# Performance work log

Measured on AMD Instinct MI355X. Metric: run time of the kernel, lower is better.

The kernel has to match this reference:

```python
import jax, jax.numpy as jnp
import numpy as np

B, N, K, CLS = 256, 15, 520, 800  # batch, points per streamline, k+k_global, classes
EPS = 1e-5


def _bn(x, g, b, m, v, axis=1):
    # eval-mode BatchNorm with running stats
    shape = [1] * x.ndim
    shape[axis] = -1
    rs = lambda a: a.reshape(shape)
    return rs(g) * (x - rs(m)) * jax.lax.rsqrt(rs(v) + EPS) + rs(b)


def setup_inputs():
    key = jax.random.key(0)
    kit = iter(jax.random.split(key, 24))
    nk = lambda: next(kit)
    p = {}
    p["pts"] = jax.random.normal(nk(), (B, N, 3), jnp.float32)
    p["label"] = jax.random.randint(nk(), (B,), 0, CLS)
    p["info_point_set"] = jax.random.normal(nk(), (B, K, N, 3), jnp.float32)

    def lin(cout, cin):
        w = jax.random.normal(nk(), (cout, cin), jnp.float32) * (1.0 / np.sqrt(cin))
        return w, jnp.zeros((cout,), jnp.float32)

    def bn(c):
        return (jnp.ones((c,), jnp.float32), jnp.zeros((c,), jnp.float32),
                jax.random.normal(nk(), (c,), jnp.float32) * 0.05,
                jnp.ones((c,), jnp.float32))

    p["w_info"], p["b_info"] = lin(64, 6)
    p["g_info"], p["be_info"], p["m_info"], p["v_info"] = bn(64)
    p["w2"], p["b2"] = lin(128, 64)
    p["g2"], p["be2"], p["m2"], p["v2"] = bn(128)
    p["w3"], p["b3"] = lin(1024, 128)
    p["g3"], p["be3"], p["m3"], p["v3"] = bn(1024)
    p["wf1"], p["bf1"] = lin(512, 1024)
    p["gf1"], p["bef1"], p["mf1"], p["vf1"] = bn(512)
    p["wf2"], p["bf2"] = lin(256, 512)
    p["gf2"], p["bef2"], p["mf2"], p["vf2"] = bn(256)
    p["wf3"], p["bf3"] = lin(CLS, 256)
    return p


def reference(pts, label, info_point_set,
              w_info, b_info, g_info, be_info, m_info, v_info,
              w2, b2, g2, be2, m2, v2,
              w3, b3, g3, be3, m3, v3,
              wf1, bf1, gf1, bef1, mf1, vf1,
              wf2, bf2, gf2, bef2, mf2, vf2,
              wf3, bf3):
    x = jnp.transpose(pts, (0, 2, 1))                      # [B,3,N]
    ips = jnp.transpose(info_point_set, (0, 3, 2, 1))      # [B,3,N,K]
    xr = jnp.broadcast_to(x[..., None], ips.shape)         # [B,3,N,K]
    h = jnp.concatenate([ips - xr, xr], axis=1)            # [B,6,N,K]
    h = jnp.einsum('oc,bcnk->bonk', w_info, h) + b_info[None, :, None, None]
    h = jax.nn.relu(_bn(h, g_info, be_info, m_info, v_info))
    h = jnp.max(h, axis=-1)                                # [B,64,N]  (max over neighbors)
    h2 = jax.nn.relu(_bn(jnp.einsum('oc,bcn->bon', w2, h) + b2[None, :, None],
                         g2, be2, m2, v2))                 # [B,128,N]
    h3 = _bn(jnp.einsum('oc,bcn->bon', w3, h2) + b3[None, :, None],
             g3, be3, m3, v3)                              # [B,1024,N]
    g = jnp.max(h3, axis=2)                                # [B,1024] global max-pool
    f1 = jax.nn.relu(_bn(g @ wf1.T + bf1, gf1, bef1, mf1, vf1, axis=1))
    f2 = jax.nn.relu(_bn(f1 @ wf2.T + bf2, gf2, bef2, mf2, vf2, axis=1))  # dropout identity (eval)
    ret = f2 @ wf3.T + bf3                                 # [B,CLS]
    return (ret, f2)
```

## Files before the change

kernel.cpp:

```cpp
#include <hip/hip_runtime.h>
#include <math.h>

#define EPS 1e-5f

typedef __attribute__((ext_vector_type(8))) short short8v;
typedef __attribute__((ext_vector_type(4))) float f32x4;
typedef __attribute__((ext_vector_type(16))) float f32x16;

__device__ __forceinline__ unsigned short bf16r(float x) {
    unsigned u = __float_as_uint(x);
    return (unsigned short)((u + 0x7FFFu + ((u >> 16) & 1u)) >> 16);
}
__device__ __forceinline__ float bf2f(unsigned short h) {
    return __uint_as_float(((unsigned)h) << 16);
}
__device__ __forceinline__ unsigned packhl(float x) {
    const unsigned short h = bf16r(x);
    const unsigned short l = bf16r(x - bf2f(h));
    return (unsigned)h | ((unsigned)l << 16);
}

__global__ __launch_bounds__(256) void k_pre(
    const float* __restrict__ w3, const float* __restrict__ b3,
    const float* __restrict__ g3, const float* __restrict__ be3,
    const float* __restrict__ m3, const float* __restrict__ v3,
    const float* __restrict__ w2, const float* __restrict__ b2,
    const float* __restrict__ g2, const float* __restrict__ be2,
    const float* __restrict__ m2, const float* __restrict__ v2,
    const float* __restrict__ w_info, const float* __restrict__ b_info,
    const float* __restrict__ g_info, const float* __restrict__ be_info,
    const float* __restrict__ m_info, const float* __restrict__ v_info,
    const float* __restrict__ bf1, const float* __restrict__ gf1,
    const float* __restrict__ bef1, const float* __restrict__ mf1,
    const float* __restrict__ vf1,
    const float* __restrict__ bf2, const float* __restrict__ gf2,
    const float* __restrict__ bef2, const float* __restrict__ mf2,
    const float* __restrict__ vf2,
    const float* __restrict__ wf1, const float* __restrict__ wf2,
    unsigned short* __restrict__ Bh, unsigned short* __restrict__ Bl,
    float* __restrict__ bias3,
    float4* __restrict__ w2q, float* __restrict__ bias2,
    unsigned short* __restrict__ Bedge,
    float4* __restrict__ qTab4,
    float* __restrict__ sf1, float* __restrict__ cf1,
    float* __restrict__ sf2, float* __restrict__ cf2,
    unsigned short* __restrict__ B1h, unsigned short* __restrict__ B1l,
    unsigned short* __restrict__ B2h, unsigned short* __restrict__ B2l)
{
    const int blk = blockIdx.x, tid = threadIdx.x;
    if (blk < 64) {
        const int t = blk * 256 + tid;
        const int kt = t >> 12;
        const int nt = (t >> 6) & 63;
        const int lane = t & 63;
        const int o  = nt * 16 + (lane & 15);
        const int kb = kt * 32 + ((lane >> 4) << 3);
        const float a3 = g3[o] * rsqrtf(v3[o] + EPS);
        #pragma unroll
        for (int j = 0; j < 8; ++j) {
            const float wv = a3 * w3[(size_t)o * 128 + kb + j];
            const unsigned short hi = bf16r(wv);
            Bh[(size_t)t * 8 + j] = hi;
            Bl[(size_t)t * 8 + j] = bf16r(wv - bf2f(hi));
        }
    } else if (blk == 64) {
        for (int idx = tid; idx < 2048; idx += 256) {
            const int o2 = idx & 127, cq = idx >> 7;
            const float a2 = g2[o2] * rsqrtf(v2[o2] + EPS);
            const float4 w = *(const float4*)(w2 + (size_t)o2 * 64 + cq * 4);
            w2q[cq * 128 + o2] = make_float4(a2 * w.x, a2 * w.y, a2 * w.z, a2 * w.w);
        }
        if (tid < 128) {
            const float a2 = g2[tid] * rsqrtf(v2[tid] + EPS);
            bias2[tid] = a2 * (b2[tid] - m2[tid]) + be2[tid];
        }
    } else if (blk == 65) {
        if (tid < 128) {
            const int nt = tid >> 6, lane = tid & 63;
            const int grp = lane >> 5;
            const int o = nt * 32 + (lane & 31);
            const float a = g_info[o] * rsqrtf(v_info[o] + EPS);
            const float c0 = a * w_info[o*6+0];
            const float c1 = a * w_info[o*6+1];
            const float c2 = a * w_info[o*6+2];
            const unsigned short ch0 = bf16r(c0), ch1 = bf16r(c1), ch2 = bf16r(c2);
            const unsigned short cl0 = bf16r(c0 - bf2f(ch0));
            const unsigned short cl1 = bf16r(c1 - bf2f(ch1));
            const unsigned short cl2 = bf16r(c2 - bf2f(ch2));
            unsigned short out[8] = {0,0,0,0,0,0,0,0};
            if (grp == 0) {
                out[0]=ch0; out[1]=ch1; out[2]=ch2;
                out[3]=cl0; out[4]=cl1; out[5]=cl2;
                out[6]=ch0; out[7]=ch1;
            } else {
                out[0]=ch2;
            }
            #pragma unroll
            for (int j = 0; j < 8; ++j)
                Bedge[(size_t)(nt*64 + lane)*8 + j] = out[j];
        }
        if (tid < 64) {
            const int o = tid;
            const float w0 = w_info[o*6+0], w1 = w_info[o*6+1], w2c = w_info[o*6+2];
            const float w3c = w_info[o*6+3], w4 = w_info[o*6+4], w5 = w_info[o*6+5];
            const float a = g_info[o] * rsqrtf(v_info[o] + EPS);
            qTab4[o] = make_float4(a*(w3c-w0), a*(w4-w1), a*(w5-w2c),
                                   a*(b_info[o]-m_info[o]) + be_info[o]);
        }
        for (int c = tid; c < 1024; c += 256) {
            const float a3 = g3[c] * rsqrtf(v3[c] + EPS);
            bias3[c] = a3 * (b3[c] - m3[c]) + be3[c];
        }
        for (int c = tid; c < 512; c += 256) {
            const float s = gf1[c] * rsqrtf(vf1[c] + EPS);
            sf1[c] = s;
            cf1[c] = s * (bf1[c] - mf1[c]) + bef1[c];
        }
        {
            const int c = tid;
            const float s = gf2[c] * rsqrtf(vf2[c] + EPS);
            sf2[c] = s;
            cf2[c] = s * (bf2[c] - mf2[c]) + bef2[c];
        }
    } else if (blk < 322) {
        const int idx = (blk - 66) * 256 + tid;
        const int lane = idx & 63;
        const int nt = (idx >> 6) & 15;
        const int kt = idx >> 10;
        const int n  = nt * 32 + (lane & 31);
        const int kb = kt * 16 + ((lane >> 5) << 3);
        #pragma unroll
        for (int j = 0; j < 8; ++j) {
            const float wv = wf1[(size_t)n * 1024 + kb + j];
            const unsigned short hi = bf16r(wv);
            B1h[(size_t)idx * 8 + j] = hi;
            B1l[(size_t)idx * 8 + j] = bf16r(wv - bf2f(hi));
        }
    } else {
        const int idx = (blk - 322) * 256 + tid;
        const int lane = idx & 63;
        const int nt = (idx >> 6) & 7;
        const int kt = idx >> 9;
        const int n  = nt * 32 + (lane & 31);
        const int kb = kt * 16 + ((lane >> 5) << 3);
        #pragma unroll
        for (int j = 0; j < 8; ++j) {
            const float wv = wf2[(size_t)n * 512 + kb + j];
            const unsigned short hi = bf16r(wv);
            B2h[(size_t)idx * 8 + j] = hi;
            B2l[(size_t)idx * 8 + j] = bf16r(wv - bf2f(hi));
        }
    }
}

__global__ __launch_bounds__(512) void k_edgeS3(
    const float* __restrict__ pts,
    const float* __restrict__ info,
    const unsigned short* __restrict__ Bedge,
    const float4* __restrict__ qTab4,
    const float4* __restrict__ w2q,
    const float* __restrict__ bias2,
    const unsigned short* __restrict__ Bh,
    const unsigned short* __restrict__ Bl,
    const float* __restrict__ bias3,
    unsigned short* __restrict__ ghi,
    unsigned short* __restrict__ glo)
{
    __shared__ unsigned dsb[23400];
    __shared__ float h1s[960];
    __shared__ unsigned short h2hL[2048];
    __shared__ unsigned short h2lL[2048];

    const int tid = threadIdx.x;
    const int b = blockIdx.x;

    {
        const float4* src = (const float4*)(info + (size_t)b * 23400);
        uint4* dst = (uint4*)dsb;
        for (int i = tid; i < 5850; i += 512) {
            const float4 v = src[i];
            uint4 pv;
            pv.x = packhl(v.x); pv.y = packhl(v.y);
            pv.z = packhl(v.z); pv.w = packhl(v.w);
            dst[i] = pv;
        }
    }
    __syncthreads();

    const int wave = tid >> 6, lane = tid & 63;
    const int la = lane & 31;
    const bool hiHalf = lane >= 32;

    {
        short8v bfrag0 = *(const short8v*)(Bedge + (size_t)(0*64 + lane)*8);
        short8v bfrag1 = *(const short8v*)(Bedge + (size_t)(1*64 + lane)*8);

        const f32x16 zero16 = {0.f,0.f,0.f,0.f,0.f,0.f,0.f,0.f,
                               0.f,0.f,0.f,0.f,0.f,0.f,0.f,0.f};

        for (int n = wave; n < 15; n += 8) {
            float m0 = -INFINITY, m1 = -INFINITY;

            #pragma unroll 1
            for (int mt = 0; mt < 17; ++mt) {
                int row = mt*32 + la;
                row = row > 519 ? 519 : row;
                const unsigned* p = dsb + row*45 + n*3;
                int4 ai;
                if (!hiHalf) {
                    const unsigned w0 = p[0], w1 = p[1], w2 = p[2];
                    ai.x = (int)((w0 & 0xFFFFu) | (w1 << 16));
                    ai.y = (int)((w2 & 0xFFFFu) | (w0 << 16));
                    ai.z = (int)((w1 & 0xFFFFu) | (w2 << 16));
                    ai.w = (int)((w0 >> 16) | (w1 & 0xFFFF0000u));
                } else {
                    const unsigned w2 = p[2];
                    ai.x = (int)(w2 >> 16);
                    ai.y = 0; ai.z = 0; ai.w = 0;
                }
                const short8v afrag = *(short8v*)&ai;
                const f32x16 r0 = __builtin_amdgcn_mfma_f32_32x32x16_bf16(afrag, bfrag0, zero16, 0,0,0);
                const f32x16 r1 = __builtin_amdgcn_mfma_f32_32x32x16_bf16(afrag, bfrag1, zero16, 0,0,0);
                #pragma unroll
                for (int c = 0; c < 16; ++c) {
                    m0 = fmaxf(m0, r0[c]);
                    m1 = fmaxf(m1, r1[c]);
                }
            }
            m0 = fmaxf(m0, __shfl_xor(m0, 32));
            m1 = fmaxf(m1, __shfl_xor(m1, 32));

            if (lane < 32) {
                const float x0 = pts[b*45 + n*3 + 0];
                const float x1 = pts[b*45 + n*3 + 1];
                const float x2 = pts[b*45 + n*3 + 2];
                {
                    const int o = lane;
                    const float4 qv = qTab4[o];
                    const float bias = fmaf(qv.x, x0, fmaf(qv.y, x1, fmaf(qv.z, x2, qv.w)));
                    h1s[n*64 + o] = fmaxf(m0 + bias, 0.f);
                }
                {
                    const int o = 32 + lane;
                    const float4 qv = qTab4[o];
                    const float bias = fmaf(qv.x, x0, fmaf(qv.y, x1, fmaf(qv.z, x2, qv.w)));
                    h1s[n*64 + o] = fmaxf(m1 + bias, 0.f);
                }
            }
        }
    }
    __syncthreads();

    for (int idx = tid; idx < 2048; idx += 512) {
        const int o2 = idx & 127, n = idx >> 7;
        float val = 0.f;
        if (n < 15) {
            float acc = 0.f;
            #pragma unroll
            for (int cq = 0; cq < 16; ++cq) {
                const float4 h4 = *(const float4*)(&h1s[n*64 + cq*4]);
                const float4 w4 = w2q[cq*128 + o2];
                acc = fmaf(w4.x, h4.x, fmaf(w4.y, h4.y,
                      fmaf(w4.z, h4.z, fmaf(w4.w, h4.w, acc))));
            }
            val = fmaxf(acc + bias2[o2], 0.f);
        }
        const unsigned short hi = bf16r(val);
        const unsigned short lo = bf16r(val - bf2f(hi));
        h2hL[idx] = hi;
        h2lL[idx] = lo;
    }
    __syncthreads();

    {
        const int arow = lane & 15, agrp = lane >> 4;

        short8v ahi[4], alo[4];
        {
            const unsigned short* Ab = h2hL + arow*128 + agrp*8;
            const unsigned short* Al = h2lL + arow*128 + agrp*8;
            #pragma unroll
            for (int kt = 0; kt < 4; ++kt) {
                ahi[kt] = *(const short8v*)(Ab + kt*32);
                alo[kt] = *(const short8v*)(Al + kt*32);
            }
        }

        for (int ntl = 0; ntl < 8; ++ntl) {
            const int nt = wave * 8 + ntl;
            f32x4 a0 = {0.f, 0.f, 0.f, 0.f};
            f32x4 a1 = a0, a2 = a0;
            #pragma unroll
            for (int kt = 0; kt < 4; ++kt) {
                const size_t off = (((size_t)kt*64 + nt)*64 + lane) * 8;
                const short8v bh = *(const short8v*)(Bh + off);
                const short8v bl = *(const short8v*)(Bl + off);
                a0 = __builtin_amdgcn_mfma_f32_16x16x32_bf16(ahi[kt], bh, a0, 0, 0, 0);
                a1 = __builtin_amdgcn_mfma_f32_16x16x32_bf16(ahi[kt], bl, a1, 0, 0, 0);
                a2 = __builtin_amdgcn_mfma_f32_16x16x32_bf16(alo[kt], bh, a2, 0, 0, 0);
            }
            const float r0 = a0[0] + a1[0] + a2[0];
            const float r1 = a0[1] + a1[1] + a2[1];
            const float r2 = a0[2] + a1[2] + a2[2];
            const float r3 = a0[3] + a1[3] + a2[3];
            float m = fmaxf(fmaxf(r0, r1), r2);
            if (agrp != 3) m = fmaxf(m, r3);
            m = fmaxf(m, __shfl_xor(m, 16));
            m = fmaxf(m, __shfl_xor(m, 32));
            if (lane < 16) {
                const float val = m + bias3[nt*16 + lane];
                const unsigned short hi = bf16r(val);
                ghi[(size_t)b*1024 + nt*16 + lane] = hi;
                glo[(size_t)b*1024 + nt*16 + lane] = bf16r(val - bf2f(hi));
            }
        }
    }
}

__global__ __launch_bounds__(256) void k_fc1m(
    const unsigned short* __restrict__ gh,
    const unsigned short* __restrict__ gl,
    const unsigned short* __restrict__ B1h,
    const unsigned short* __restrict__ B1l,
    const float* __restrict__ sf1, const float* __restrict__ cf1,
    unsigned short* __restrict__ f1h,
    unsigned short* __restrict__ f1l)
{
    __shared__ float part[4][32][33];

    const int tid = threadIdx.x;
    const int bm = blockIdx.x * 32, bn = blockIdx.y * 32;
    const int wave = tid >> 6, lane = tid & 63;
    const int m = bm + (lane & 31);
    const int kgrp = (lane >> 5) << 3;

    f32x16 acc = {0.f,0.f,0.f,0.f,0.f,0.f,0.f,0.f,
                  0.f,0.f,0.f,0.f,0.f,0.f,0.f,0.f};

    for (int kt = wave*16; kt < wave*16 + 16; ++kt) {
        const int kb = kt*16 + kgrp;
        const short8v ah = *(const short8v*)(gh + (size_t)m*1024 + kb);
        const short8v al = *(const short8v*)(gl + (size_t)m*1024 + kb);
        const size_t boff = ((size_t)kt*1024 + blockIdx.y*64 + lane) * 8;
        const short8v bh = *(const short8v*)(B1h + boff);
        const short8v bl = *(const short8v*)(B1l + boff);
        acc = __builtin_amdgcn_mfma_f32_32x32x16_bf16(ah, bh, acc, 0,0,0);
        acc = __builtin_amdgcn_mfma_f32_32x32x16_bf16(ah, bl, acc, 0,0,0);
        acc = __builtin_amdgcn_mfma_f32_32x32x16_bf16(al, bh, acc, 0,0,0);
    }
    {
        const int n = lane & 31, mhl = (lane >> 5) << 2;
        #pragma unroll
        for (int reg = 0; reg < 16; ++reg) {
            const int mrow = (reg & 3) + 8*(reg >> 2) + mhl;
            part[wave][mrow][n] = acc[reg];
        }
    }
    __syncthreads();

    for (int i = tid; i < 1024; i += 256) {
        const int lm = i >> 5, ln = i & 31;
        const float sum = part[0][lm][ln] + part[1][lm][ln]
                        + part[2][lm][ln] + part[3][lm][ln];
        const int ch = bn + ln;
        const float val = fmaxf(fmaf(sf1[ch], sum, cf1[ch]), 0.f);
        const unsigned short hi = bf16r(val);
        f1h[(size_t)(bm + lm)*512 + ch] = hi;
        f1l[(size_t)(bm + lm)*512 + ch] = bf16r(val - bf2f(hi));
    }
}

__global__ __launch_bounds__(256) void k_fc2m(
    const unsigned short* __restrict__ f1h,
    const unsigned short* __restrict__ f1l,
    const unsigned short* __restrict__ B2h,
    const unsigned short* __restrict__ B2l,
    const float* __restrict__ sf2, const float* __restrict__ cf2,
    float* __restrict__ f2out)
{
    __shared__ float part[4][32][33];

    const int tid = threadIdx.x;
    const int bm = blockIdx.x * 32, bn = blockIdx.y * 32;
    const int wave = tid >> 6, lane = tid & 63;
    const int m = bm + (lane & 31);
    const int kgrp = (lane >> 5) << 3;

    f32x16 acc = {0.f,0.f,0.f,0.f,0.f,0.f,0.f,0.f,
                  0.f,0.f,0.f,0.f,0.f,0.f,0.f,0.f};

    for (int kt = wave*8; kt < wave*8 + 8; ++kt) {
        const int kb = kt*16 + kgrp;
        const short8v ah = *(const short8v*)(f1h + (size_t)m*512 + kb);
        const short8v al = *(const short8v*)(f1l + (size_t)m*512 + kb);
        const size_t boff = ((size_t)kt*512 + blockIdx.y*64 + lane) * 8;
        const short8v bh = *(const short8v*)(B2h + boff);
        const short8v bl = *(const short8v*)(B2l + boff);
        acc = __builtin_amdgcn_mfma_f32_32x32x16_bf16(ah, bh, acc, 0,0,0);
        acc = __builtin_amdgcn_mfma_f32_32x32x16_bf16(ah, bl, acc, 0,0,0);
        acc = __builtin_amdgcn_mfma_f32_32x32x16_bf16(al, bh, acc, 0,0,0);
    }
    {
        const int n = lane & 31, mhl = (lane >> 5) << 2;
        #pragma unroll
        for (int reg = 0; reg < 16; ++reg) {
            const int mrow = (reg & 3) + 8*(reg >> 2) + mhl;
            part[wave][mrow][n] = acc[reg];
        }
    }
    __syncthreads();

    for (int i = tid; i < 1024; i += 256) {
        const int lm = i >> 5, ln = i & 31;
        const float sum = part[0][lm][ln] + part[1][lm][ln]
                        + part[2][lm][ln] + part[3][lm][ln];
        const int ch = bn + ln;
        f2out[(size_t)(bm + lm)*256 + ch] =
            fmaxf(fmaf(sf2[ch], sum, cf2[ch]), 0.f);
    }
}

__global__ __launch_bounds__(256) void k_fc3(
    const float* __restrict__ A, const float* __restrict__ W,
    const float* __restrict__ bias, float* __restrict__ C, int K, int Nc)
{
    __shared__ float As[32][36];
    __shared__ float Ws[32][36];

    const int tid = threadIdx.x;
    const int bm = blockIdx.x * 32, bn = blockIdx.y * 32;
    const int ml = (tid >> 4) * 2, nl = (tid & 15) * 2;
    const int row = tid >> 3, kq = (tid & 7) * 4;

    float acc00 = 0.f, acc01 = 0.f, acc10 = 0.f, acc11 = 0.f;

    for (int k0 = 0; k0 < K; k0 += 32) {
        const float4 av = *(const float4*)(A + (size_t)(bm + row) * K + k0 + kq);
        const float4 wv = *(const float4*)(W + (size_t)(bn + row) * K + k0 + kq);
        __syncthreads();
        *(float4*)(&As[row][kq]) = av;
        *(float4*)(&Ws[row][kq]) = wv;
        __syncthreads();
        const float4* a0p = (const float4*)(&As[ml][0]);
        const float4* a1p = (const float4*)(&As[ml + 1][0]);
        const float4* b0p = (const float4*)(&Ws[nl][0]);
        const float4* b1p = (const float4*)(&Ws[nl + 1][0]);
        #pragma unroll
        for (int q = 0; q < 8; ++q) {
            const float4 a0 = a0p[q], a1 = a1p[q], b0 = b0p[q], b1 = b1p[q];
            acc00 = fmaf(a0.x, b0.x, fmaf(a0.y, b0.y, fmaf(a0.z, b0.z, fmaf(a0.w, b0.w, acc00))));
            acc01 = fmaf(a0.x, b1.x, fmaf(a0.y, b1.y, fmaf(a0.z, b1.z, fmaf(a0.w, b1.w, acc01))));
            acc10 = fmaf(a1.x, b0.x, fmaf(a1.y, b0.y, fmaf(a1.z, b0.z, fmaf(a1.w, b0.w, acc10))));
            acc11 = fmaf(a1.x, b1.x, fmaf(a1.y, b1.y, fmaf(a1.z, b1.z, fmaf(a1.w, b1.w, acc11))));
        }
    }

    const int n0 = bn + nl, n1 = n0 + 1;
    float* cr0 = C + (size_t)(bm + ml) * Nc + n0;
    cr0[0] = acc00 + bias[n0]; cr0[1] = acc01 + bias[n1];
    float* cr1 = C + (size_t)(bm + ml + 1) * Nc + n0;
    cr1[0] = acc10 + bias[n0]; cr1[1] = acc11 + bias[n1];
}

extern "C" void kernel_launch(void* const* d_in, const int* in_sizes, int n_in,
                              void* d_out, int out_size, void* d_ws, size_t ws_size,
                              hipStream_t stream)
{
    const float* pts     = (const float*)d_in[0];
    const float* info    = (const float*)d_in[2];
    const float* w_info  = (const float*)d_in[3];
    const float* b_info  = (const float*)d_in[4];
    const float* g_info  = (const float*)d_in[5];
    const float* be_info = (const float*)d_in[6];
    const float* m_info  = (const float*)d_in[7];
    const float* v_info  = (const float*)d_in[8];
    const float* w2      = (const float*)d_in[9];
    const float* b2      = (const float*)d_in[10];
    const float* g2      = (const float*)d_in[11];
    const float* be2     = (const float*)d_in[12];
    const float* m2      = (const float*)d_in[13];
    const float* v2      = (const float*)d_in[14];
    const float* w3      = (const float*)d_in[15];
    const float* b3      = (const float*)d_in[16];
    const float* g3      = (const float*)d_in[17];
    const float* be3     = (const float*)d_in[18];
    const float* m3      = (const float*)d_in[19];
    const float* v3      = (const float*)d_in[20];
    const float* wf1     = (const float*)d_in[21];
    const float* bf1     = (const float*)d_in[22];
    const float* gf1     = (const float*)d_in[23];
    const float* bef1    = (const float*)d_in[24];
    const float* mf1     = (const float*)d_in[25];
    const float* vf1     = (const float*)d_in[26];
    const float* wf2     = (const float*)d_in[27];
    const float* bf2     = (const float*)d_in[28];
    const float* gf2     = (const float*)d_in[29];
    const float* bef2    = (const float*)d_in[30];
    const float* mf2     = (const float*)d_in[31];
    const float* vf2     = (const float*)d_in[32];
    const float* wf3     = (const float*)d_in[33];
    const float* bf3     = (const float*)d_in[34];

    float* ws = (float*)d_ws;
    unsigned short* ghi   = (unsigned short*)(ws + 0);
    unsigned short* glo   = (unsigned short*)(ws + 131072);
    unsigned short* f1h   = (unsigned short*)(ws + 262144);
    unsigned short* f1l   = (unsigned short*)(ws + 327680);
    unsigned short* B1h   = (unsigned short*)(ws + 393216);
    unsigned short* B1l   = (unsigned short*)(ws + 655360);
    unsigned short* B2h   = (unsigned short*)(ws + 917504);
    unsigned short* B2l   = (unsigned short*)(ws + 983040);
    unsigned short* Bh    = (unsigned short*)(ws + 1277952);
    unsigned short* Bl    = (unsigned short*)(ws + 1343488);
    float*          bias3 = ws + 1409024;
    float4*         w2q   = (float4*)(ws + 1410048);
    float*          bias2 = ws + 1418240;
    float4*         qTab4 = (float4*)(ws + 1418624);
    float*          sf1   = ws + 1418880;
    float*          cf1   = ws + 1419392;
    float*          sf2   = ws + 1419904;
    float*          cf2   = ws + 1420160;
    unsigned short* Bedge = (unsigned short*)(ws + 1420416);

    float* ret = (float*)d_out;
    float* f2  = ret + 256 * 800;

    k_pre<<<386, 256, 0, stream>>>(
        w3, b3, g3, be3, m3, v3,
        w2, b2, g2, be2, m2, v2,
        w_info, b_info, g_info, be_info, m_info, v_info,
        bf1, gf1, bef1, mf1, vf1,
        bf2, gf2, bef2, mf2, vf2,
        wf1, wf2,
        Bh, Bl, bias3, w2q, bias2, Bedge, qTab4, sf1, cf1, sf2, cf2,
        B1h, B1l, B2h, B2l);

    k_edgeS3<<<256, 512, 0, stream>>>(pts, info, Bedge, qTab4,
                                      w2q, bias2, Bh, Bl, bias3, ghi, glo);

    k_fc1m<<<dim3(8, 16), 256, 0, stream>>>(ghi, glo, B1h, B1l,
                                            sf1, cf1, f1h, f1l);

    k_fc2m<<<dim3(8, 8), 256, 0, stream>>>(f1h, f1l, B2h, B2l,
                                           sf2, cf2, f2);

    k_fc3<<<dim3(8, 25), 256, 0, stream>>>(f2, wf3, bf3, ret, 256, 800);
}
```

Before: 62.02 us.

## Move fc3 to split-bf16 MFMA and prefetch LDS rows in edge loop

The final 256x800x256 linear layer moves from a scalar FP32 LDS-tiled GEMM to a 3-pass split-bf16 MFMA kernel. wf3 is pre-packed into hi/lo bf16 fragments in k_pre, and fc2 now also emits hi/lo bf16 copies of f2. Separately, the edge-conv loop software-prefetches the next row's LDS words one iteration ahead and rewrites the max reduction as a tree. This cuts the fc3 FP32 FMA work and hides LDS latency, but adds extra prep blocks, extra stores of f2, and more register pressure in the edge kernel.

```diff
diff --git a/kernel.cpp b/kernel.cpp
--- a/kernel.cpp
+++ b/kernel.cpp
@@ -37,6 +37,7 @@
     const float* __restrict__ bef2, const float* __restrict__ mf2,
     const float* __restrict__ vf2,
     const float* __restrict__ wf1, const float* __restrict__ wf2,
+    const float* __restrict__ wf3,
     unsigned short* __restrict__ Bh, unsigned short* __restrict__ Bl,
     float* __restrict__ bias3,
     float4* __restrict__ w2q, float* __restrict__ bias2,
@@ -45,7 +46,8 @@
     float* __restrict__ sf1, float* __restrict__ cf1,
     float* __restrict__ sf2, float* __restrict__ cf2,
     unsigned short* __restrict__ B1h, unsigned short* __restrict__ B1l,
-    unsigned short* __restrict__ B2h, unsigned short* __restrict__ B2l)
+    unsigned short* __restrict__ B2h, unsigned short* __restrict__ B2l,
+    unsigned short* __restrict__ B3h, unsigned short* __restrict__ B3l)
 {
     const int blk = blockIdx.x, tid = threadIdx.x;
     if (blk < 64) {
@@ -136,7 +138,7 @@
             B1h[(size_t)idx * 8 + j] = hi;
             B1l[(size_t)idx * 8 + j] = bf16r(wv - bf2f(hi));
         }
-    } else {
+    } else if (blk < 386) {
         const int idx = (blk - 322) * 256 + tid;
         const int lane = idx & 63;
         const int nt = (idx >> 6) & 7;
@@ -149,6 +151,21 @@
             const unsigned short hi = bf16r(wv);
             B2h[(size_t)idx * 8 + j] = hi;
             B2l[(size_t)idx * 8 + j] = bf16r(wv - bf2f(hi));
+        }
+    } else {
+        const int idx = (blk - 386) * 256 + tid;
+        const int lane = idx & 63;
+        const int g6 = idx >> 6;
+        const int nt = g6 % 25;
+        const int kt = g6 / 25;
+        const int n  = nt * 32 + (lane & 31);
+        const int kb = kt * 16 + ((lane >> 5) << 3);
+        #pragma unroll
+        for (int j = 0; j < 8; ++j) {
+            const float wv = wf3[(size_t)n * 256 + kb + j];
+            const unsigned short hi = bf16r(wv);
+            B3h[(size_t)idx * 8 + j] = hi;
+            B3l[(size_t)idx * 8 + j] = bf16r(wv - bf2f(hi));
         }
     }
 }
@@ -200,21 +217,32 @@
 
         for (int n = wave; n < 15; n += 8) {
             float m0 = -INFINITY, m1 = -INFINITY;
+            const unsigned* pb = dsb + n*3;
+
+            unsigned w0 = 0, w1 = 0, w2 = 0;
+            {
+                const unsigned* p = pb + la*45;
+                if (!hiHalf) { w0 = p[0]; w1 = p[1]; }
+                w2 = p[2];
+            }
 
             #pragma unroll 1
             for (int mt = 0; mt < 17; ++mt) {
-                int row = mt*32 + la;
-                row = row > 519 ? 519 : row;
-                const unsigned* p = dsb + row*45 + n*3;
+                unsigned nw0 = 0, nw1 = 0, nw2 = 0;
+                if (mt < 16) {
+                    int nrow = (mt+1)*32 + la;
+                    nrow = nrow > 519 ? 519 : nrow;
+                    const unsigned* p = pb + nrow*45;
+                    if (!hiHalf) { nw0 = p[0]; nw1 = p[1]; }
+                    nw2 = p[2];
+                }
                 int4 ai;
                 if (!hiHalf) {
-                    const unsigned w0 = p[0], w1 = p[1], w2 = p[2];
                     ai.x = (int)((w0 & 0xFFFFu) | (w1 << 16));
                     ai.y = (int)((w2 & 0xFFFFu) | (w0 << 16));
                     ai.z = (int)((w1 & 0xFFFFu) | (w2 << 16));
                     ai.w = (int)((w0 >> 16) | (w1 & 0xFFFF0000u));
                 } else {
-                    const unsigned w2 = p[2];
                     ai.x = (int)(w2 >> 16);
                     ai.y = 0; ai.z = 0; ai.w = 0;
                 }
@@ -222,10 +250,13 @@
                 const f32x16 r0 = __builtin_amdgcn_mfma_f32_32x32x16_bf16(afrag, bfrag0, zero16, 0,0,0);
                 const f32x16 r1 = __builtin_amdgcn_mfma_f32_32x32x16_bf16(afrag, bfrag1, zero16, 0,0,0);
                 #pragma unroll
-                for (int c = 0; c < 16; ++c) {
-                    m0 = fmaxf(m0, r0[c]);
-                    m1 = fmaxf(m1, r1[c]);
+                for (int c = 0; c < 16; c += 4) {
+                    m0 = fmaxf(m0, fmaxf(fmaxf(r0[c], r0[c+1]),
+                                         fmaxf(r0[c+2], r0[c+3])));
+                    m1 = fmaxf(m1, fmaxf(fmaxf(r1[c], r1[c+1]),
+                                         fmaxf(r1[c+2], r1[c+3])));
                 }
+                w0 = nw0; w1 = nw1; w2 = nw2;
             }
             m0 = fmaxf(m0, __shfl_xor(m0, 32));
             m1 = fmaxf(m1, __shfl_xor(m1, 32));
@@ -376,7 +407,9 @@
     const unsigned short* __restrict__ B2h,
     const unsigned short* __restrict__ B2l,
     const float* __restrict__ sf2, const float* __restrict__ cf2,
-    float* __restrict__ f2out)
+    float* __restrict__ f2out,
+    unsigned short* __restrict__ f2h,
+    unsigned short* __restrict__ f2l)
 {
     __shared__ float part[4][32][33];
 
@@ -415,51 +448,62 @@
         const float sum = part[0][lm][ln] + part[1][lm][ln]
                         + part[2][lm][ln] + part[3][lm][ln];
         const int ch = bn + ln;
-        f2out[(size_t)(bm + lm)*256 + ch] =
-            fmaxf(fmaf(sf2[ch], sum, cf2[ch]), 0.f);
-    }
-}
-
-__global__ __launch_bounds__(256) void k_fc3(
-    const float* __restrict__ A, const float* __restrict__ W,
-    const float* __restrict__ bias, float* __restrict__ C, int K, int Nc)
+        const float val = fmaxf(fmaf(sf2[ch], sum, cf2[ch]), 0.f);
+        const size_t o = (size_t)(bm + lm)*256 + ch;
+        f2out[o] = val;
+        const unsigned short hi = bf16r(val);
+        f2h[o] = hi;
+        f2l[o] = bf16r(val - bf2f(hi));
+    }
+}
+
+__global__ __launch_bounds__(256) void k_fc3m(
+    const unsigned short* __restrict__ f2h,
+    const unsigned short* __restrict__ f2l,
+    const unsigned short* __restrict__ B3h,
+    const unsigned short* __restrict__ B3l,
+    const float* __restrict__ bias,
+    float* __restrict__ C)
 {
-    __shared__ float As[32][36];
-    __shared__ float Ws[32][36];
+    __shared__ float part[4][32][33];
 
     const int tid = threadIdx.x;
-    const int bm = blockIdx.x * 32, bn = blockIdx.y * 32;
-    const int ml = (tid >> 4) * 2, nl = (tid & 15) * 2;
-    const int row = tid >> 3, kq = (tid & 7) * 4;
-
-    float acc00 = 0.f, acc01 = 0.f, acc10 = 0.f, acc11 = 0.f;
-
-    for (int k0 = 0; k0 < K; k0 += 32) {
-        const float4 av = *(const float4*)(A + (size_t)(bm + row) * K + k0 + kq);
-        const float4 wv = *(const float4*)(W + (size_t)(bn + row) * K + k0 + kq);
-        __syncthreads();
-        *(float4*)(&As[row][kq]) = av;
-        *(float4*)(&Ws[row][kq]) = wv;
-        __syncthreads();
-        const float4* a0p = (const float4*)(&As[ml][0]);
-        const float4* a1p = (const float4*)(&As[ml + 1][0]);
-        const float4* b0p = (const float4*)(&Ws[nl][0]);
-        const float4* b1p = (const float4*)(&Ws[nl + 1][0]);
-        #pragma unroll
-        for (int q = 0; q < 8; ++q) {
-            const float4 a0 = a0p[q], a1 = a1p[q], b0 = b0p[q], b1 = b1p[q];
-            acc00 = fmaf(a0.x, b0.x, fmaf(a0.y, b0.y, fmaf(a0.z, b0.z, fmaf(a0.w, b0.w, acc00))));
-            acc01 = fmaf(a0.x, b1.x, fmaf(a0.y, b1.y, fmaf(a0.z, b1.z, fmaf(a0.w, b1.w, acc01))));
-            acc10 = fmaf(a1.x, b0.x, fmaf(a1.y, b0.y, fmaf(a1.z, b0.z, fmaf(a1.w, b0.w, acc10))));
-            acc11 = fmaf(a1.x, b1.x, fmaf(a1.y, b1.y, fmaf(a1.z, b1.z, fmaf(a1.w, b1.w, acc11))));
-        }
-    }
-
-    const int n0 = bn + nl, n1 = n0 + 1;
-    float* cr0 = C + (size_t)(bm + ml) * Nc + n0;
-    cr0[0] = acc00 + bias[n0]; cr0[1] = acc01 + bias[n1];
-    float* cr1 = C + (size_t)(bm + ml + 1) * Nc + n0;
-    cr1[0] = acc10 + bias[n0]; cr1[1] = acc11 + bias[n1];
+    const int bm = blockIdx.x * 32;
+    const int wave = tid >> 6, lane = tid & 63;
+    const int m = bm + (lane & 31);
+    const int kgrp = (lane >> 5) << 3;
+
+    f32x16 acc = {0.f,0.f,0.f,0.f,0.f,0.f,0.f,0.f,
+                  0.f,0.f,0.f,0.f,0.f,0.f,0.f,0.f};
+
+    for (int kt = wave*4; kt < wave*4 + 4; ++kt) {
+        const int kb = kt*16 + kgrp;
+        const short8v ah = *(const short8v*)(f2h + (size_t)m*256 + kb);
+        const short8v al = *(const short8v*)(f2l + (size_t)m*256 + kb);
+        const size_t boff = (((size_t)kt*25 + blockIdx.y)*64 + lane) * 8;
+        const short8v bh = *(const short8v*)(B3h + boff);
+        const short8v bl = *(const short8v*)(B3l + boff);
+        acc = __builtin_amdgcn_mfma_f32_32x32x16_bf16(ah, bh, acc, 0,0,0);
+        acc = __builtin_amdgcn_mfma_f32_32x32x16_bf16(ah, bl, acc, 0,0,0);
+        acc = __builtin_amdgcn_mfma_f32_32x32x16_bf16(al, bh, acc, 0,0,0);
+    }
+    {
+        const int n = lane & 31, mhl = (lane >> 5) << 2;
+        #pragma unroll
+        for (int reg = 0; reg < 16; ++reg) {
+            const int mrow = (reg & 3) + 8*(reg >> 2) + mhl;
+            part[wave][mrow][n] = acc[reg];
+        }
+    }
+    __syncthreads();
+
+    for (int i = tid; i < 1024; i += 256) {
+        const int lm = i >> 5, ln = i & 31;
+        const float sum = part[0][lm][ln] + part[1][lm][ln]
+                        + part[2][lm][ln] + part[3][lm][ln];
+        const int ch = blockIdx.y * 32 + ln;
+        C[(size_t)(bm + lm)*800 + ch] = sum + bias[ch];
+    }
 }
 
 extern "C" void kernel_launch(void* const* d_in, const int* in_sizes, int n_in,
@@ -504,12 +548,16 @@
     float* ws = (float*)d_ws;
     unsigned short* ghi   = (unsigned short*)(ws + 0);
     unsigned short* glo   = (unsigned short*)(ws + 131072);
+    unsigned short* f2h   = (unsigned short*)(ws + 0);
+    unsigned short* f2l   = (unsigned short*)(ws + 32768);
     unsigned short* f1h   = (unsigned short*)(ws + 262144);
     unsigned short* f1l   = (unsigned short*)(ws + 327680);
     unsigned short* B1h   = (unsigned short*)(ws + 393216);
     unsigned short* B1l   = (unsigned short*)(ws + 655360);
     unsigned short* B2h   = (unsigned short*)(ws + 917504);
     unsigned short* B2l   = (unsigned short*)(ws + 983040);
+    unsigned short* B3h   = (unsigned short*)(ws + 1048576);
+    unsigned short* B3l   = (unsigned short*)(ws + 1150976);
     unsigned short* Bh    = (unsigned short*)(ws + 1277952);
     unsigned short* Bl    = (unsigned short*)(ws + 1343488);
     float*          bias3 = ws + 1409024;
@@ -525,15 +573,15 @@
     float* ret = (float*)d_out;
     float* f2  = ret + 256 * 800;
 
-    k_pre<<<386, 256, 0, stream>>>(
+    k_pre<<<486, 256, 0, stream>>>(
         w3, b3, g3, be3, m3, v3,
         w2, b2, g2, be2, m2, v2,
         w_info, b_info, g_info, be_info, m_info, v_info,
         bf1, gf1, bef1, mf1, vf1,
         bf2, gf2, bef2, mf2, vf2,
-        wf1, wf2,
+        wf1, wf2, wf3,
         Bh, Bl, bias3, w2q, bias2, Bedge, qTab4, sf1, cf1, sf2, cf2,
-        B1h, B1l, B2h, B2l);
+        B1h, B1l, B2h, B2l, B3h, B3l);
 
     k_edgeS3<<<256, 512, 0, stream>>>(pts, info, Bedge, qTab4,
                                       w2q, bias2, Bh, Bl, bias3, ghi, glo);
@@ -542,7 +590,7 @@
                                             sf1, cf1, f1h, f1l);
 
     k_fc2m<<<dim3(8, 8), 256, 0, stream>>>(f1h, f1l, B2h, B2l,
-                                           sf2, cf2, f2);
-
-    k_fc3<<<dim3(8, 25), 256, 0, stream>>>(f2, wf3, bf3, ret, 256, 800);
-}
+                                           sf2, cf2, f2, f2h, f2l);
+
+    k_fc3m<<<dim3(8, 25), 256, 0, stream>>>(f2h, f2l, B3h, B3l, bf3, ret);
+}
```

After: 60.16 us. 1.03x faster.
